# Performance work log

Measured on AMD Instinct MI355X. Metric: run time of the kernel, lower is better.

Reference implementation:

```python
import jax, jax.numpy as jnp
import numpy as np

JITTER = 0.1

def se_kernel(X, X2, length_scale):
    # K[i,j] = exp(-||x_i - x2_j||^2 / length_scale^2)   (no 1/2 factor, as in source)
    Xs = X / length_scale
    X2s = X2 / length_scale
    d2 = (jnp.sum(Xs * Xs, axis=1)[:, None]
          - 2.0 * Xs @ X2s.T
          + jnp.sum(X2s * X2s, axis=1)[None, :])
    return jnp.exp(-d2)

def kron(A, B):
    # kronecker(A, B) as in source: einsum 'ab,cd->acbd' then reshape
    return jnp.einsum('ab,cd->acbd', A, B).reshape(A.shape[0] * B.shape[0], A.shape[1] * B.shape[1])

def setup_inputs() -> dict:
    key = jax.random.key(0)
    ks = jax.random.split(key, 5)
    return {
        'space_coordinates': jax.random.normal(ks[0], (150, 3), dtype=jnp.float32),
        'time_coordinates': jax.random.normal(ks[1], (40, 1), dtype=jnp.float32),
        'stData': jax.random.normal(ks[2], (150, 40), dtype=jnp.float32),
        'test_space_coordinates': jax.random.normal(ks[3], (200, 3), dtype=jnp.float32),
        'test_time_coordinates': jax.random.normal(ks[4], (30, 1), dtype=jnp.float32),
        'log_latlong_length_scale': jnp.log(jnp.asarray(1.0, dtype=jnp.float32)),
        'log_elevation_length_scale': jnp.log(jnp.asarray(1.0, dtype=jnp.float32)),
        'log_time_length_scale': jnp.log(jnp.asarray(0.25, dtype=jnp.float32)),
        'log_noise_variance': jnp.log(jnp.asarray(0.1, dtype=jnp.float32)),
        'log_signal_variance': jnp.log(jnp.asarray(1.0, dtype=jnp.float32)),
    }

def reference(space_coordinates, time_coordinates, stData,
              test_space_coordinates, test_time_coordinates,
              log_latlong_length_scale, log_elevation_length_scale,
              log_time_length_scale, log_noise_variance, log_signal_variance):
    ll = jnp.exp(log_latlong_length_scale)
    le = jnp.exp(log_elevation_length_scale)
    lt = jnp.exp(log_time_length_scale)
    Ns = space_coordinates.shape[0]
    Nt = time_coordinates.shape[0]

    # ---- update(): build sigma_inverse and alpha via Kronecker eigendecomposition ----
    spatial_K = (se_kernel(space_coordinates[:, 0:2], space_coordinates[:, 0:2], ll)
                 * se_kernel(space_coordinates[:, 2:3], space_coordinates[:, 2:3], le)
                 + JITTER * jnp.eye(Ns, dtype=space_coordinates.dtype))
    temporal_K = (se_kernel(time_coordinates, time_coordinates, lt)
                  + JITTER * jnp.eye(Nt, dtype=time_coordinates.dtype))
    ws, Vs = jnp.linalg.eigh(spatial_K)
    wt, Vt = jnp.linalg.eigh(temporal_K)
    V = kron(Vt, Vs)                                   # [N, N], N = Nt*Ns
    w = jnp.einsum('a,b->ab', wt, ws).reshape(-1)      # eigenvalues of kron kernel
    inv = 1.0 / (w + jnp.exp(log_noise_variance))
    sigma_inverse = (V * inv[None, :]) @ V.T           # V diag(inv) V^T
    alpha = sigma_inverse @ stData.T.reshape(-1, 1)    # [N, 1]

    # ---- forward ----
    test_spatial = (se_kernel(test_space_coordinates[:, 0:2], space_coordinates[:, 0:2], ll)
                    * se_kernel(test_space_coordinates[:, 2:3], space_coordinates[:, 2:3], le))
    test_temporal = se_kernel(test_time_coordinates, time_coordinates, lt)
    Kst = kron(test_temporal, test_spatial)            # [M, N], M = Mt*Ms
    yPred = Kst @ alpha                                # [M, 1]
    # fused row-wise quadratic form: diag(Kst sigma_inverse Kst^T)
    yVar = jnp.exp(log_signal_variance) - jnp.sum((Kst @ sigma_inverse) * Kst, axis=1)
    Mt = test_time_coordinates.shape[0]
    Ms = test_space_coordinates.shape[0]
    yPred = yPred.reshape(Mt, Ms).T                    # [Ms, Mt]
    yVar = yVar.reshape(Mt, Ms).T                      # [Ms, Mt]
    return (yPred, yVar)
```

## Files before the change

### kernel.cpp

```cpp
#include <hip/hip_runtime.h>
#include <math.h>

#define NS 150
#define LDW 152
#define NPACK 11848
#define NT 40
#define MS 200
#define MT 30
#define N_SWEEPS 6
#define ROUNDS (N_SWEEPS*(NT-1))
#define JITTER 0.1f
#define NTHR 512

#define OFF_MP    0
#define OFF_PR    47392
#define OFF_INVS  52256
#define OFF_DVS   52288
#define OFF_SCS   52896
#define OFF_TSCS  54704
#define OFF_QV    57104
#define OFF_RV    57904
#define OFF_GV    58704
#define OFF_ACOL  59304
#define OFF_WTJ   59424
#define SMEM_BYTES 59440
#define OFF_A2    0
#define OFF_VTS   13120
#define OFF_PRM   20160
#define OFF_TCS   22720

__device__ __forceinline__ int rs_off(int r) {
    int g = r >> 2, rm = r & 3;
    return LDW * r - 8 * g * (g - 1) - 4 * rm * g;
}

__device__ __forceinline__ void jac_params(const float (*A)[NT+1], float4* dst,
                                           int i, int rr) {
    int i0 = i, i1 = NT - 1 - i;
    int p = (i0 == 0) ? 0 : ((i0 - 1 + rr) % (NT - 1)) + 1;
    int q = ((i1 - 1 + rr) % (NT - 1)) + 1;
    if (p > q) { int tsw = p; p = q; q = tsw; }
    float app = A[p][p], aqq = A[q][q], apq = A[p][q];
    float c, s;
    if (apq == 0.0f) { c = 1.0f; s = 0.0f; }
    else {
        float tau = (aqq - app) / (2.0f * apq);
        float tt = ((tau >= 0.0f) ? 1.0f : -1.0f) / (fabsf(tau) + sqrtf(1.0f + tau*tau));
        c = rsqrtf(1.0f + tt*tt);
        s = tt * c;
    }
    dst[i] = make_float4(c, s, __int_as_float(p), __int_as_float(q));
}

__global__ void __launch_bounds__(NTHR, 1) gp_block(
        const float* __restrict__ sc,  const float* __restrict__ tc,
        const float* __restrict__ st,  const float* __restrict__ tsc,
        const float* __restrict__ ttc,
        const float* __restrict__ lll, const float* __restrict__ lle,
        const float* __restrict__ llt, const float* __restrict__ lnv,
        const float* __restrict__ lsv, float* __restrict__ out) {
    __shared__ __align__(16) char smem[SMEM_BYTES];
    int j = blockIdx.x, tid = threadIdx.x;

    auto A2   = (float (*)[NT][NT+1])(smem + OFF_A2);
    auto Vts  = (float (*)[44])(smem + OFF_VTS);
    auto prm  = (float4 (*)[NT/2])(smem + OFF_PRM);
    float* tcs  = (float*)(smem + OFF_TCS);
    float* gv   = (float*)(smem + OFF_GV);
    float* Acol = (float*)(smem + OFF_ACOL);
    float* wtjs = (float*)(smem + OFF_WTJ);
    float* scs  = (float*)(smem + OFF_SCS);
    float* tscs = (float*)(smem + OFF_TSCS);

    float ilt2 = expf(-2.0f * llt[0]);
    if (tid < NT) tcs[tid] = tc[tid];
    for (int t = tid; t < NS*3; t += NTHR) scs[t] = sc[t];
    for (int t = tid; t < MS*3; t += NTHR) tscs[t] = tsc[t];
    __syncthreads();
    for (int idx = tid; idx < NT*NT; idx += NTHR) {
        int i = idx / NT, jj = idx - i*NT;
        float dt = tcs[i] - tcs[jj];
        float v = expf(-dt*dt*ilt2);
        if (i == jj) v += JITTER;
        A2[0][i][jj] = v;
    }
    for (int idx = tid; idx < NT*44; idx += NTHR) {
        int jr = idx / 44, k = idx - jr*44;
        Vts[jr][k] = (jr == k) ? 1.0f : 0.0f;
    }
    __syncthreads();
    int wave = tid >> 6, lane = tid & 63;
    for (int rd = 0; rd < ROUNDS; ++rd) {
        int cur = rd & 1, nxt = cur ^ 1;
        float4* wp = prm[wave];
        if (lane < NT/2) jac_params(A2[cur], wp, lane, rd % (NT - 1));
        __builtin_amdgcn_wave_barrier();
        for (int t = tid; t < 600; t += NTHR) {
            if (t < 400) {
                int bi = t / 20, bj = t - bi*20;
                float4 Pi = wp[bi], Pj = wp[bj];
                int pi = __float_as_int(Pi.z), qi = __float_as_int(Pi.w);
                int pj = __float_as_int(Pj.z), qj = __float_as_int(Pj.w);
                float ci = Pi.x, si = Pi.y, cj = Pj.x, sj = Pj.y;
                float a00 = A2[cur][pi][pj], a01 = A2[cur][pi][qj];
                float a10 = A2[cur][qi][pj], a11 = A2[cur][qi][qj];
                float b00 = ci*a00 - si*a10, b01 = ci*a01 - si*a11;
                float b10 = si*a00 + ci*a10, b11 = si*a01 + ci*a11;
                A2[nxt][pi][pj] = cj*b00 - sj*b01; A2[nxt][pi][qj] = sj*b00 + cj*b01;
                A2[nxt][qi][pj] = cj*b10 - sj*b11; A2[nxt][qi][qj] = sj*b10 + cj*b11;
            } else {
                int u2 = t - 400;
                int pr = u2 / 10, ch = (u2 - pr*10) << 2;
                float4 P = wp[pr];
                int pj = __float_as_int(P.z), qj = __float_as_int(P.w);
                float c = P.x, s = P.y;
                float4 vp = *(float4*)&Vts[pj][ch];
                float4 vq = *(float4*)&Vts[qj][ch];
                float4 np, nq;
                np.x = c*vp.x - s*vq.x; nq.x = s*vp.x + c*vq.x;
                np.y = c*vp.y - s*vq.y; nq.y = s*vp.y + c*vq.y;
                np.z = c*vp.z - s*vq.z; nq.z = s*vp.z + c*vq.z;
                np.w = c*vp.w - s*vq.w; nq.w = s*vp.w + c*vq.w;
                *(float4*)&Vts[pj][ch] = np;
                *(float4*)&Vts[qj][ch] = nq;
            }
        }
        __syncthreads();
    }
    const int fin = ROUNDS & 1;
    if (tid == 0) wtjs[0] = A2[fin][j][j];
    for (int s = tid; s < NS; s += NTHR) {
        const float4* va = (const float4*)&Vts[j][0];
        const float4* sa = (const float4*)&st[s*NT];
        float acc = 0.0f;
        #pragma unroll
        for (int c4 = 0; c4 < NT/4; ++c4) {
            float4 a = va[c4], b = sa[c4];
            acc += a.x*b.x + a.y*b.y + a.z*b.z + a.w*b.w;
        }
        gv[s] = acc;
    }
    if (tid < MT) {
        float ttv = ttc[tid];
        float acc = 0.0f;
        for (int t = 0; t < NT; ++t) {
            float dt = ttv - tcs[t];
            acc += expf(-dt*dt*ilt2) * Vts[j][t];
        }
        Acol[tid] = acc;
    }
    __syncthreads();

    float* Mp   = (float*)(smem + OFF_MP);
    auto   Pr   = (float (*)[LDW])(smem + OFF_PR);
    float* invs = (float*)(smem + OFF_INVS);
    float* dvs  = (float*)(smem + OFF_DVS);
    float* qv   = (float*)(smem + OFF_QV);
    float* Rv   = (float*)(smem + OFF_RV);
    float wtj = wtjs[0];
    float nv = expf(lnv[0]);
    float ill2 = expf(-2.0f * lll[0]);
    float ile2 = expf(-2.0f * lle[0]);
    for (int idx = tid; idx < NS*LDW; idx += NTHR) {
        int r = idx / LDW, c = idx - r*LDW;
        int rbase = r & ~3;
        if (c < rbase) continue;
        float v;
        if (c < NS) {
            float d0 = scs[r*3+0] - scs[c*3+0];
            float d1 = scs[r*3+1] - scs[c*3+1];
            float d2 = scs[r*3+2] - scs[c*3+2];
            v = wtj * expf(-((d0*d0 + d1*d1)*ill2 + d2*d2*ile2));
            if (c == r) v += wtj * JITTER + nv;
        } else if (c == NS) {
            v = gv[r];
        } else {
            v = 0.0f;
        }
        Mp[rs_off(r) + c - rbase] = v;
    }
    __syncthreads();
    for (int k0 = 0; k0 < NS - 1; k0 += 8) {
        int P = NS - k0; if (P > 8) P = 8;
        int W4 = (LDW - k0) >> 2;
        if (tid < W4) {
            int off[8];
            #pragma unroll
            for (int i = 0; i < 8; ++i)
                off[i] = (i < P) ? (rs_off(k0 + i) - ((i >= 4) ? 4 : 0)) : 0;
            float Bm[8][8];
            #pragma unroll
            for (int i = 0; i < 8; ++i) {
                #pragma unroll
                for (int c = 0; c < 8; ++c)
                    Bm[i][c] = (i < P && c >= i) ? Mp[off[i] + c]
                                                 : ((c == i) ? 1.0f : 0.0f);
            }
            float Lf[8][8]; float iv[8];
            #pragma unroll
            for (int k = 0; k < 8; ++k) {
                iv[k] = 1.0f / Bm[k][k];
                #pragma unroll
                for (int i = k + 1; i < 8; ++i) {
                    float l = Bm[k][i] * iv[k];
                    Lf[i][k] = l;
                    #pragma unroll
                    for (int c = i; c < 8; ++c) Bm[i][c] -= l * Bm[k][c];
                }
            }
            if (tid == 0) {
                #pragma unroll
                for (int i = 0; i < 8; ++i) invs[i] = iv[i];
            }
            int C = tid << 2;
            float4 m[8];
            #pragma unroll
            for (int i = 0; i < 8; ++i) {
                bool ok = (i < P) && (i < 4 || C >= 4);
                m[i] = ok ? *(float4*)&Mp[off[i] + C] : make_float4(0,0,0,0);
            }
            #pragma unroll
            for (int i = 1; i < 8; ++i) {
                #pragma unroll
                for (int k = 0; k < i; ++k) {
                    float l = Lf[i][k];
                    m[i].x -= l*m[k].x; m[i].y -= l*m[k].y;
                    m[i].z -= l*m[k].z; m[i].w -= l*m[k].w;
                }
            }
            #pragma unroll
            for (int i = 0; i < 8; ++i) *(float4*)&Pr[i][C] = m[i];
        }
        __syncthreads();
        for (int r = k0 + 1 + tid; r < NS; r += NTHR) {
            int rc = r - k0;
            float f[8];
            #pragma unroll
            for (int i = 0; i < 8; ++i)
                f[i] = (rc > i && i < P) ? Pr[i][rc] * invs[i] : 0.0f;
            int rbase = r & ~3;
            int ro = rs_off(r) - rbase;
            for (int C = rbase; C < LDW; C += 4) {
                int pc = C - k0;
                float4 v = *(float4*)&Mp[ro + C];
                #pragma unroll
                for (int i = 0; i < 8; ++i) {
                    float4 p = *(float4*)&Pr[i][pc];
                    v.x -= f[i]*p.x; v.y -= f[i]*p.y;
                    v.z -= f[i]*p.z; v.w -= f[i]*p.w;
                }
                *(float4*)&Mp[ro + C] = v;
            }
        }
        __syncthreads();
    }
    for (int r = tid; r < NS; r += NTHR)
        dvs[r] = rsqrtf(Mp[rs_off(r) + r - (r & ~3)]);
    __syncthreads();
    for (int idx = tid; idx < NS*LDW; idx += NTHR) {
        int r = idx / LDW, c = idx - r*LDW;
        int rbase = r & ~3;
        if (c < rbase) continue;
        int t = rs_off(r) + c - rbase;
        float dvr = dvs[r];
        if (c == r) Mp[t] = dvr;
        else if (c > r) Mp[t] *= dvr;
    }
    __syncthreads();
    if (tid < MS) {
        float tx = tscs[tid*3+0], ty = tscs[tid*3+1], tz = tscs[tid*3+2];
        float u[LDW];
        #pragma unroll
        for (int k = 0; k < NS; ++k) {
            float d0 = tx - scs[k*3+0];
            float d1 = ty - scs[k*3+1];
            float d2 = tz - scs[k*3+2];
            u[k] = expf(-((d0*d0 + d1*d1)*ill2 + d2*d2*ile2));
        }
        u[150] = 0.0f; u[151] = 0.0f;
        float qa = 0.0f, ra = 0.0f;
        #pragma unroll
        for (int k = 0; k < NS; ++k) {
            const int base = rs_off(k) - (k & ~3);
            float uk = u[k] * Mp[base + k];
            qa += uk * uk;
            ra += uk * Mp[base + 150];
            const int kp = k + 1;
            const int ka = (kp + 3) & ~3;
            #pragma unroll
            for (int t = kp; t < ((ka < NS) ? ka : NS); ++t)
                u[t] -= Mp[base + t] * uk;
            #pragma unroll
            for (int t = ka; t < NS; t += 4) {
                float4 w = *(const float4*)&Mp[base + t];
                u[t+0] -= w.x * uk; u[t+1] -= w.y * uk;
                u[t+2] -= w.z * uk; u[t+3] -= w.w * uk;
            }
        }
        qv[tid] = qa;
        Rv[tid] = ra;
    }
    __syncthreads();

    float sigv = expf(lsv[0]);
    for (int idx = tid; idx < MS*MT; idx += NTHR) {
        int is = idx / MT, it = idx - is*MT;
        float a = Acol[it];
        atomicAdd(&out[idx], a * Rv[is]);
        float c2 = -a * a * qv[is];
        if (j == 0) c2 += sigv;
        atomicAdd(&out[MS*MT + idx], c2);
    }
}

extern "C" void kernel_launch(void* const* d_in, const int* in_sizes, int n_in,
                              void* d_out, int out_size, void* d_ws, size_t ws_size,
                              hipStream_t stream) {
    const float* sc  = (const float*)d_in[0];
    const float* tc  = (const float*)d_in[1];
    const float* st  = (const float*)d_in[2];
    const float* tsc = (const float*)d_in[3];
    const float* ttc = (const float*)d_in[4];
    const float* lll = (const float*)d_in[5];
    const float* lle = (const float*)d_in[6];
    const float* llt = (const float*)d_in[7];
    const float* lnv = (const float*)d_in[8];
    const float* lsv = (const float*)d_in[9];
    float* out = (float*)d_out;

    hipMemsetAsync(out, 0, (size_t)out_size * sizeof(float), stream);
    hipLaunchKernelGGL(gp_block, dim3(NT), dim3(NTHR), 0, stream,
                       sc, tc, st, tsc, ttc, lll, lle, llt, lnv, lsv, out);
}
```

Baseline: 418.4 us.

## Run Jacobi eigensolve on one wave while other waves precompute spatial kernel

The 40x40 Jacobi eigendecomposition moves from all 512 threads, which paid a block-wide __syncthreads every round and used a double-buffered A matrix, to a single wave. That wave updates A in place and synchronises only with wave barriers. The other seven waves meanwhile fill the unscaled spatial kernel into the packed matrix for rows from PREROW onward, and a later pass scales those entries by the eigenvalue and computes rows below PREROW directly. This removes the per-round block barriers and overlaps the serial eigensolve with kernel construction. The cost is fewer lanes doing the rotation work, and the in-place rotation relies on the parallel Jacobi pairs being disjoint within a round.

```diff
diff --git a/kernel.cpp b/kernel.cpp
--- a/kernel.cpp
+++ b/kernel.cpp
@@ -11,8 +11,13 @@
 #define ROUNDS (N_SWEEPS*(NT-1))
 #define JITTER 0.1f
 #define NTHR 512
+#define PREROW 45
 
 #define OFF_MP    0
+#define OFF_JA    0
+#define OFF_JV    6560
+#define OFF_JP    13600
+#define OFF_JT    13920
 #define OFF_PR    47392
 #define OFF_INVS  52256
 #define OFF_DVS   52288
@@ -24,10 +29,6 @@
 #define OFF_ACOL  59304
 #define OFF_WTJ   59424
 #define SMEM_BYTES 59440
-#define OFF_A2    0
-#define OFF_VTS   13120
-#define OFF_PRM   20160
-#define OFF_TCS   22720
 
 __device__ __forceinline__ int rs_off(int r) {
     int g = r >> 2, rm = r & 3;
@@ -61,11 +62,13 @@
         const float* __restrict__ lsv, float* __restrict__ out) {
     __shared__ __align__(16) char smem[SMEM_BYTES];
     int j = blockIdx.x, tid = threadIdx.x;
-
-    auto A2   = (float (*)[NT][NT+1])(smem + OFF_A2);
-    auto Vts  = (float (*)[44])(smem + OFF_VTS);
-    auto prm  = (float4 (*)[NT/2])(smem + OFF_PRM);
-    float* tcs  = (float*)(smem + OFF_TCS);
+    int wave = tid >> 6, lane = tid & 63;
+
+    auto Aj   = (float (*)[NT+1])(smem + OFF_JA);
+    auto Vts  = (float (*)[44])(smem + OFF_JV);
+    float4* wp  = (float4*)(smem + OFF_JP);
+    float* tcs  = (float*)(smem + OFF_JT);
+    float* Mp   = (float*)(smem + OFF_MP);
     float* gv   = (float*)(smem + OFF_GV);
     float* Acol = (float*)(smem + OFF_ACOL);
     float* wtjs = (float*)(smem + OFF_WTJ);
@@ -73,6 +76,8 @@
     float* tscs = (float*)(smem + OFF_TSCS);
 
     float ilt2 = expf(-2.0f * llt[0]);
+    float ill2 = expf(-2.0f * lll[0]);
+    float ile2 = expf(-2.0f * lle[0]);
     if (tid < NT) tcs[tid] = tc[tid];
     for (int t = tid; t < NS*3; t += NTHR) scs[t] = sc[t];
     for (int t = tid; t < MS*3; t += NTHR) tscs[t] = tsc[t];
@@ -82,35 +87,34 @@
         float dt = tcs[i] - tcs[jj];
         float v = expf(-dt*dt*ilt2);
         if (i == jj) v += JITTER;
-        A2[0][i][jj] = v;
+        Aj[i][jj] = v;
     }
     for (int idx = tid; idx < NT*44; idx += NTHR) {
         int jr = idx / 44, k = idx - jr*44;
         Vts[jr][k] = (jr == k) ? 1.0f : 0.0f;
     }
     __syncthreads();
-    int wave = tid >> 6, lane = tid & 63;
-    for (int rd = 0; rd < ROUNDS; ++rd) {
-        int cur = rd & 1, nxt = cur ^ 1;
-        float4* wp = prm[wave];
-        if (lane < NT/2) jac_params(A2[cur], wp, lane, rd % (NT - 1));
-        __builtin_amdgcn_wave_barrier();
-        for (int t = tid; t < 600; t += NTHR) {
-            if (t < 400) {
+
+    if (wave == 0) {
+        for (int rd = 0; rd < ROUNDS; ++rd) {
+            int rr = rd % (NT - 1);
+            if (lane < NT/2) jac_params(Aj, wp, lane, rr);
+            __builtin_amdgcn_wave_barrier();
+            for (int t = lane; t < 400; t += 64) {
                 int bi = t / 20, bj = t - bi*20;
                 float4 Pi = wp[bi], Pj = wp[bj];
                 int pi = __float_as_int(Pi.z), qi = __float_as_int(Pi.w);
                 int pj = __float_as_int(Pj.z), qj = __float_as_int(Pj.w);
                 float ci = Pi.x, si = Pi.y, cj = Pj.x, sj = Pj.y;
-                float a00 = A2[cur][pi][pj], a01 = A2[cur][pi][qj];
-                float a10 = A2[cur][qi][pj], a11 = A2[cur][qi][qj];
+                float a00 = Aj[pi][pj], a01 = Aj[pi][qj];
+                float a10 = Aj[qi][pj], a11 = Aj[qi][qj];
                 float b00 = ci*a00 - si*a10, b01 = ci*a01 - si*a11;
                 float b10 = si*a00 + ci*a10, b11 = si*a01 + ci*a11;
-                A2[nxt][pi][pj] = cj*b00 - sj*b01; A2[nxt][pi][qj] = sj*b00 + cj*b01;
-                A2[nxt][qi][pj] = cj*b10 - sj*b11; A2[nxt][qi][qj] = sj*b10 + cj*b11;
-            } else {
-                int u2 = t - 400;
-                int pr = u2 / 10, ch = (u2 - pr*10) << 2;
+                Aj[pi][pj] = cj*b00 - sj*b01; Aj[pi][qj] = sj*b00 + cj*b01;
+                Aj[qi][pj] = cj*b10 - sj*b11; Aj[qi][qj] = sj*b10 + cj*b11;
+            }
+            for (int t = lane; t < 200; t += 64) {
+                int pr = t / 10, ch = (t - pr*10) << 2;
                 float4 P = wp[pr];
                 int pj = __float_as_int(P.z), qj = __float_as_int(P.w);
                 float c = P.x, s = P.y;
@@ -124,11 +128,23 @@
                 *(float4*)&Vts[pj][ch] = np;
                 *(float4*)&Vts[qj][ch] = nq;
             }
-        }
-        __syncthreads();
-    }
-    const int fin = ROUNDS & 1;
-    if (tid == 0) wtjs[0] = A2[fin][j][j];
+            __builtin_amdgcn_wave_barrier();
+        }
+    } else {
+        for (int idx = PREROW*LDW + (tid - 64); idx < NS*LDW; idx += NTHR - 64) {
+            int r = idx / LDW, c = idx - r*LDW;
+            int rbase = r & ~3;
+            if (c < rbase || c >= NS) continue;
+            float d0 = scs[r*3+0] - scs[c*3+0];
+            float d1 = scs[r*3+1] - scs[c*3+1];
+            float d2 = scs[r*3+2] - scs[c*3+2];
+            Mp[rs_off(r) + c - rbase] =
+                expf(-((d0*d0 + d1*d1)*ill2 + d2*d2*ile2));
+        }
+    }
+    __syncthreads();
+
+    if (tid == 0) wtjs[0] = Aj[j][j];
     for (int s = tid; s < NS; s += NTHR) {
         const float4* va = (const float4*)&Vts[j][0];
         const float4* sa = (const float4*)&st[s*NT];
@@ -151,35 +167,34 @@
     }
     __syncthreads();
 
-    float* Mp   = (float*)(smem + OFF_MP);
+    float wtj = wtjs[0];
+    float nv = expf(lnv[0]);
+    for (int idx = tid; idx < NS*LDW; idx += NTHR) {
+        int r = idx / LDW, c = idx - r*LDW;
+        int rbase = r & ~3;
+        if (c < rbase) continue;
+        int t = rs_off(r) + c - rbase;
+        if (c == NS) { Mp[t] = gv[r]; continue; }
+        if (c > NS)  { Mp[t] = 0.0f; continue; }
+        float v;
+        if (r < PREROW) {
+            float d0 = scs[r*3+0] - scs[c*3+0];
+            float d1 = scs[r*3+1] - scs[c*3+1];
+            float d2 = scs[r*3+2] - scs[c*3+2];
+            v = wtj * expf(-((d0*d0 + d1*d1)*ill2 + d2*d2*ile2));
+        } else {
+            v = wtj * Mp[t];
+        }
+        if (c == r) v += wtj * JITTER + nv;
+        Mp[t] = v;
+    }
+    __syncthreads();
+
     auto   Pr   = (float (*)[LDW])(smem + OFF_PR);
     float* invs = (float*)(smem + OFF_INVS);
     float* dvs  = (float*)(smem + OFF_DVS);
     float* qv   = (float*)(smem + OFF_QV);
     float* Rv   = (float*)(smem + OFF_RV);
-    float wtj = wtjs[0];
-    float nv = expf(lnv[0]);
-    float ill2 = expf(-2.0f * lll[0]);
-    float ile2 = expf(-2.0f * lle[0]);
-    for (int idx = tid; idx < NS*LDW; idx += NTHR) {
-        int r = idx / LDW, c = idx - r*LDW;
-        int rbase = r & ~3;
-        if (c < rbase) continue;
-        float v;
-        if (c < NS) {
-            float d0 = scs[r*3+0] - scs[c*3+0];
-            float d1 = scs[r*3+1] - scs[c*3+1];
-            float d2 = scs[r*3+2] - scs[c*3+2];
-            v = wtj * expf(-((d0*d0 + d1*d1)*ill2 + d2*d2*ile2));
-            if (c == r) v += wtj * JITTER + nv;
-        } else if (c == NS) {
-            v = gv[r];
-        } else {
-            v = 0.0f;
-        }
-        Mp[rs_off(r) + c - rbase] = v;
-    }
-    __syncthreads();
     for (int k0 = 0; k0 < NS - 1; k0 += 8) {
         int P = NS - k0; if (P > 8) P = 8;
         int W4 = (LDW - k0) >> 2;
```

Measured after the change: 890.2 us. 2.13x slower.

## Split triangular-solve epilogue into separate kernel spread across more blocks

Applied to the files above, without the earlier changes.

The per-time-eigenvalue Cholesky factor is now written to workspace, and a second kernel runs the test-point triangular solves with 160 blocks of 64 threads, each handling 50 test points, instead of 200 threads inside each of only 40 blocks. This spreads the register-heavy, serial solve across more CUs. Each thread also accumulates its outputs directly rather than staging through shared memory. The cost is an extra kernel launch plus global round trips of the packed factor, about 47 KB per block.

```diff
diff --git a/kernel.cpp b/kernel.cpp
--- a/kernel.cpp
+++ b/kernel.cpp
@@ -17,13 +17,10 @@
 #define OFF_INVS  52256
 #define OFF_DVS   52288
 #define OFF_SCS   52896
-#define OFF_TSCS  54704
-#define OFF_QV    57104
-#define OFF_RV    57904
-#define OFF_GV    58704
-#define OFF_ACOL  59304
-#define OFF_WTJ   59424
-#define SMEM_BYTES 59440
+#define OFF_GV    54704
+#define OFF_ACOL  55304
+#define OFF_WTJ   55424
+#define SMEM_BYTES 55440
 #define OFF_A2    0
 #define OFF_VTS   13120
 #define OFF_PRM   20160
@@ -52,13 +49,12 @@
     dst[i] = make_float4(c, s, __int_as_float(p), __int_as_float(q));
 }
 
-__global__ void __launch_bounds__(NTHR, 1) gp_block(
+__global__ void __launch_bounds__(NTHR, 1) gp_factor(
         const float* __restrict__ sc,  const float* __restrict__ tc,
-        const float* __restrict__ st,  const float* __restrict__ tsc,
-        const float* __restrict__ ttc,
+        const float* __restrict__ st,  const float* __restrict__ ttc,
         const float* __restrict__ lll, const float* __restrict__ lle,
         const float* __restrict__ llt, const float* __restrict__ lnv,
-        const float* __restrict__ lsv, float* __restrict__ out) {
+        float* __restrict__ Ug, float* __restrict__ AcolG) {
     __shared__ __align__(16) char smem[SMEM_BYTES];
     int j = blockIdx.x, tid = threadIdx.x;
 
@@ -70,12 +66,10 @@
     float* Acol = (float*)(smem + OFF_ACOL);
     float* wtjs = (float*)(smem + OFF_WTJ);
     float* scs  = (float*)(smem + OFF_SCS);
-    float* tscs = (float*)(smem + OFF_TSCS);
 
     float ilt2 = expf(-2.0f * llt[0]);
     if (tid < NT) tcs[tid] = tc[tid];
     for (int t = tid; t < NS*3; t += NTHR) scs[t] = sc[t];
-    for (int t = tid; t < MS*3; t += NTHR) tscs[t] = tsc[t];
     __syncthreads();
     for (int idx = tid; idx < NT*NT; idx += NTHR) {
         int i = idx / NT, jj = idx - i*NT;
@@ -155,8 +149,6 @@
     auto   Pr   = (float (*)[LDW])(smem + OFF_PR);
     float* invs = (float*)(smem + OFF_INVS);
     float* dvs  = (float*)(smem + OFF_DVS);
-    float* qv   = (float*)(smem + OFF_QV);
-    float* Rv   = (float*)(smem + OFF_RV);
     float wtj = wtjs[0];
     float nv = expf(lnv[0]);
     float ill2 = expf(-2.0f * lll[0]);
@@ -267,49 +259,71 @@
         else if (c > r) Mp[t] *= dvr;
     }
     __syncthreads();
-    if (tid < MS) {
-        float tx = tscs[tid*3+0], ty = tscs[tid*3+1], tz = tscs[tid*3+2];
-        float u[LDW];
+    for (int t4 = tid * 4; t4 < NPACK; t4 += NTHR * 4)
+        *(float4*)&Ug[(size_t)j*NPACK + t4] = *(float4*)&Mp[t4];
+    if (tid < MT) AcolG[j*MT + tid] = Acol[tid];
+}
+
+__global__ void __launch_bounds__(64) trsm_ep(
+        const float* __restrict__ Ug, const float* __restrict__ AcolG,
+        const float* __restrict__ sc, const float* __restrict__ tsc,
+        const float* __restrict__ lll, const float* __restrict__ lle,
+        const float* __restrict__ lsv, float* __restrict__ out) {
+    __shared__ __align__(16) float Up[NPACK];
+    __shared__ float scs[NS*3 + 2];
+    __shared__ float AcolS[MT];
+    int bid = blockIdx.x;
+    int j = bid >> 2, grp = bid & 3;
+    int lane = threadIdx.x;
+    for (int t4 = lane * 4; t4 < NPACK; t4 += 256)
+        *(float4*)&Up[t4] = *(const float4*)&Ug[(size_t)j*NPACK + t4];
+    for (int t = lane; t < NS*3; t += 64) scs[t] = sc[t];
+    if (lane < MT) AcolS[lane] = AcolG[j*MT + lane];
+    __syncthreads();
+    float ill2 = expf(-2.0f * lll[0]);
+    float ile2 = expf(-2.0f * lle[0]);
+    int c = grp * 50 + lane;
+    bool active = (lane < 50);
+    int cc = active ? c : 0;
+    float tx = tsc[cc*3+0], ty = tsc[cc*3+1], tz = tsc[cc*3+2];
+    float u[LDW];
+    #pragma unroll
+    for (int k = 0; k < NS; ++k) {
+        float d0 = tx - scs[k*3+0];
+        float d1 = ty - scs[k*3+1];
+        float d2 = tz - scs[k*3+2];
+        u[k] = expf(-((d0*d0 + d1*d1)*ill2 + d2*d2*ile2));
+    }
+    u[150] = 0.0f; u[151] = 0.0f;
+    float qa = 0.0f, ra = 0.0f;
+    #pragma unroll
+    for (int k = 0; k < NS; ++k) {
+        const int base = rs_off(k) - (k & ~3);
+        float uk = u[k] * Up[base + k];
+        qa += uk * uk;
+        ra += uk * Up[base + 150];
+        const int kp = k + 1;
+        const int ka = (kp + 3) & ~3;
         #pragma unroll
-        for (int k = 0; k < NS; ++k) {
-            float d0 = tx - scs[k*3+0];
-            float d1 = ty - scs[k*3+1];
-            float d2 = tz - scs[k*3+2];
-            u[k] = expf(-((d0*d0 + d1*d1)*ill2 + d2*d2*ile2));
-        }
-        u[150] = 0.0f; u[151] = 0.0f;
-        float qa = 0.0f, ra = 0.0f;
+        for (int t = kp; t < ((ka < NS) ? ka : NS); ++t)
+            u[t] -= Up[base + t] * uk;
         #pragma unroll
-        for (int k = 0; k < NS; ++k) {
-            const int base = rs_off(k) - (k & ~3);
-            float uk = u[k] * Mp[base + k];
-            qa += uk * uk;
-            ra += uk * Mp[base + 150];
-            const int kp = k + 1;
-            const int ka = (kp + 3) & ~3;
-            #pragma unroll
-            for (int t = kp; t < ((ka < NS) ? ka : NS); ++t)
-                u[t] -= Mp[base + t] * uk;
-            #pragma unroll
-            for (int t = ka; t < NS; t += 4) {
-                float4 w = *(const float4*)&Mp[base + t];
-                u[t+0] -= w.x * uk; u[t+1] -= w.y * uk;
-                u[t+2] -= w.z * uk; u[t+3] -= w.w * uk;
-            }
-        }
-        qv[tid] = qa;
-        Rv[tid] = ra;
-    }
-    __syncthreads();
-
-    float sigv = expf(lsv[0]);
-    for (int idx = tid; idx < MS*MT; idx += NTHR) {
-        int is = idx / MT, it = idx - is*MT;
-        float a = Acol[it];
-        atomicAdd(&out[idx], a * Rv[is]);
-        float c2 = -a * a * qv[is];
-        if (j == 0) c2 += sigv;
-        atomicAdd(&out[MS*MT + idx], c2);
+        for (int t = ka; t < NS; t += 4) {
+            float4 w = *(const float4*)&Up[base + t];
+            u[t+0] -= w.x * uk; u[t+1] -= w.y * uk;
+            u[t+2] -= w.z * uk; u[t+3] -= w.w * uk;
+        }
+    }
+    if (active) {
+        float sigv = expf(lsv[0]);
+        #pragma unroll
+        for (int it = 0; it < MT; ++it) {
+            float a = AcolS[it];
+            atomicAdd(&out[c*MT + it], a * ra);
+            float c2 = -a * a * qa;
+            if (j == 0) c2 += sigv;
+            atomicAdd(&out[MS*MT + c*MT + it], c2);
+        }
     }
 }
 
@@ -328,7 +342,13 @@
     const float* lsv = (const float*)d_in[9];
     float* out = (float*)d_out;
 
+    float* ws    = (float*)d_ws;
+    float* Ug    = ws;
+    float* AcolG = Ug + (size_t)NT*NPACK;
+
     hipMemsetAsync(out, 0, (size_t)out_size * sizeof(float), stream);
-    hipLaunchKernelGGL(gp_block, dim3(NT), dim3(NTHR), 0, stream,
-                       sc, tc, st, tsc, ttc, lll, lle, llt, lnv, lsv, out);
-}
+    hipLaunchKernelGGL(gp_factor, dim3(NT), dim3(NTHR), 0, stream,
+                       sc, tc, st, ttc, lll, lle, llt, lnv, Ug, AcolG);
+    hipLaunchKernelGGL(trsm_ep, dim3(NT*4), dim3(64), 0, stream,
+                       Ug, AcolG, sc, tsc, lll, lle, lsv, out);
+}
```

After: 516.6 us. +23.5%, slower.
